# Kernel optimization log

Measured on AMD Instinct MI355X. Metric: run time of the kernel, lower is better.

## Reference

```python
import jax, jax.numpy as jnp
import numpy as np

H = 4          # attention heads
NEG_SLOPE = 0.2

def _gat_layer(h, src, dst, W, a_src, a_dst, b):
    # h: [N, F_in]; W: [F_in, H*D]; a_src/a_dst: [H, D]; b: [D]
    N = h.shape[0]
    D = a_src.shape[1]
    xh = (h @ W).reshape(N, H, D)                       # [N,H,D]
    al_src = jnp.einsum('nhd,hd->nh', xh, a_src)        # [N,H]
    al_dst = jnp.einsum('nhd,hd->nh', xh, a_dst)        # [N,H]
    e = jax.nn.leaky_relu(al_src[src] + al_dst[dst], NEG_SLOPE)  # [E,H]
    # segment softmax over incoming edges of each destination node
    m = jax.ops.segment_max(e, dst, num_segments=N)     # [N,H]
    ex = jnp.exp(e - m[dst])
    s = jax.ops.segment_sum(ex, dst, num_segments=N)
    alpha = ex / (s[dst] + 1e-16)                       # [E,H]
    out = jax.ops.segment_sum(xh[src] * alpha[:, :, None], dst, num_segments=N)  # [N,H,D]
    return out.mean(axis=1) + b                         # concat=False -> mean heads


def setup_inputs() -> dict:
    key = jax.random.key(0)
    ks = jax.random.split(key, 16)
    N, E, F_in, Dh = 50000, 400000, 128, 128
    inp = {
        'x': jax.random.normal(ks[0], (N, F_in), jnp.float32),
        'edge_index': jax.random.randint(ks[1], (2, E), 0, N, jnp.int64),
    }
    def glorot(k, shape):
        fan = shape[0] + shape[-1]
        return jax.random.uniform(k, shape, jnp.float32, -1.0, 1.0) * np.sqrt(6.0 / fan)
    dims = [F_in, Dh, Dh]
    for i, fin in enumerate(dims, start=1):
        inp[f'W{i}'] = glorot(ks[2 + 4 * i], (fin, H * Dh))
        inp[f'a_src{i}'] = glorot(ks[3 + 4 * i], (H, Dh))
        inp[f'a_dst{i}'] = glorot(ks[4 + 4 * i], (H, Dh))
        inp[f'b{i}'] = jnp.zeros((Dh,), jnp.float32)
    inp['Wp'] = glorot(ks[2], (Dh, Dh))
    inp['bp'] = jnp.zeros((Dh,), jnp.float32)
    return inp


def reference(x, edge_index, W1, a_src1, a_dst1, b1, W2, a_src2, a_dst2, b2,
              W3, a_src3, a_dst3, b3, Wp, bp):
    N = x.shape[0]
    loops = jnp.arange(N, dtype=edge_index.dtype)
    src = jnp.concatenate([edge_index[0], loops])   # GATConv adds self-loops
    dst = jnp.concatenate([edge_index[1], loops])
    h = x
    for W, a_s, a_d, b in ((W1, a_src1, a_dst1, b1),
                           (W2, a_src2, a_dst2, b2),
                           (W3, a_src3, a_dst3, b3)):
        h = _gat_layer(h, src, dst, W, a_s, a_d, b)
        h = jax.nn.relu(h)   # dropout is identity in eval mode
    return h @ Wp + bp
```

## Files before the change

kernel.cpp:

```cpp
#include <hip/hip_runtime.h>
#include <cstddef>
#include <cstdint>

typedef _Float16 half8 __attribute__((ext_vector_type(8)));
typedef float f32x4 __attribute__((ext_vector_type(4)));
typedef float f32x2 __attribute__((ext_vector_type(2)));
typedef unsigned short ushort_t;
typedef unsigned int uint_t;
typedef ushort_t ushort4v __attribute__((ext_vector_type(4)));
typedef float f32x4v __attribute__((ext_vector_type(4)));

#define INV_LN2 1.4426950408889634f

__device__ __forceinline__ ushort_t f_to_f16(float f) {
  _Float16 h = (_Float16)f;
  union { _Float16 h; ushort_t u; } v; v.h = h; return v.u;
}
__device__ __forceinline__ float f16_to_f(ushort_t u) {
  union { ushort_t u; _Float16 h; } v; v.u = u; return (float)v.h;
}

__global__ __launch_bounds__(64) void detect_i64_kernel(const int* __restrict__ ei,
                                                        int* __restrict__ flag) {
  if (threadIdx.x == 0) {
    int is32 = 0;
    for (int i = 1; i < 1001; i += 2) {
      if (ei[i] != 0) { is32 = 1; break; }
    }
    *flag = is32;
  }
}

__device__ __forceinline__ int load_src(const int* ei, int is32, int E, int e) {
  return is32 ? ei[e] : ei[2 * e];
}
__device__ __forceinline__ int load_dst(const int* ei, int is32, int E, int e) {
  return is32 ? ei[E + e] : ei[2 * (E + e)];
}

__global__ __launch_bounds__(256) void deg_kernel(const int* __restrict__ ei,
                                                  const int* __restrict__ flag,
                                                  int E, int N, int* __restrict__ deg) {
  int e = blockIdx.x * 256 + threadIdx.x;
  if (e >= E + N) return;
  int d = (e < E) ? load_dst(ei, *flag, E, e) : (e - E);
  atomicAdd(&deg[d], 1);
}

__global__ __launch_bounds__(256) void scan_blk_kernel(const int* __restrict__ deg,
                                                       int* __restrict__ rowptr,
                                                       int* __restrict__ bsum, int N) {
  __shared__ int buf[256];
  int b = blockIdx.x, t = threadIdx.x, i = b * 256 + t;
  int v = (i < N) ? deg[i] : 0;
  buf[t] = v;
  __syncthreads();
  for (int off = 1; off < 256; off <<= 1) {
    int add = (t >= off) ? buf[t - off] : 0;
    __syncthreads();
    buf[t] += add;
    __syncthreads();
  }
  if (i < N) rowptr[i + 1] = buf[t];
  if (t == 255) bsum[b] = buf[255];
  if (b == 0 && t == 0) rowptr[0] = 0;
}

__global__ __launch_bounds__(256) void scan_top_kernel(int* __restrict__ bsum, int NB) {
  __shared__ int buf[256];
  int t = threadIdx.x;
  int v = (t < NB) ? bsum[t] : 0;
  buf[t] = v;
  __syncthreads();
  for (int off = 1; off < 256; off <<= 1) {
    int add = (t >= off) ? buf[t - off] : 0;
    __syncthreads();
    buf[t] += add;
    __syncthreads();
  }
  if (t < NB) bsum[t] = buf[t];
}

__global__ __launch_bounds__(256) void scan_add_kernel(int* __restrict__ rowptr,
                                                       const int* __restrict__ bsum, int N) {
  int b = blockIdx.x, t = threadIdx.x, i = b * 256 + t;
  if (b > 0 && i < N) rowptr[i + 1] += bsum[b - 1];
}

__global__ __launch_bounds__(256) void fill_kernel(const int* __restrict__ ei,
                                                   const int* __restrict__ flag,
                                                   int E, int N,
                                                   const int* __restrict__ rowptr,
                                                   int* __restrict__ fillc,
                                                   int* __restrict__ colbuf) {
  int e = blockIdx.x * 256 + threadIdx.x;
  if (e >= E + N) return;
  int s, d;
  if (e < E) { int is32 = *flag; s = load_src(ei, is32, E, e); d = load_dst(ei, is32, E, e); }
  else { s = e - E; d = s; }
  int pos = atomicAdd(&fillc[d], 1);
  colbuf[rowptr[d] + pos] = s;
}

__global__ __launch_bounds__(256) void split_x16_kernel(const float* __restrict__ h,
                                                        ushort_t* __restrict__ h16,
                                                        int n) {
  int i = (blockIdx.x * 256 + threadIdx.x) * 4;
  if (i >= n) return;
  f32x4v v = *(const f32x4v*)&h[i];
  ushort4v s;
  s[0] = f_to_f16(v[0]); s[1] = f_to_f16(v[1]);
  s[2] = f_to_f16(v[2]); s[3] = f_to_f16(v[3]);
  *(ushort4v*)&h16[i] = s;
}

__global__ __launch_bounds__(256) void prep_weights_kernel(
    const float* __restrict__ W0, const float* __restrict__ W1,
    const float* __restrict__ W2, const float* __restrict__ Wp,
    ushort_t* __restrict__ wsf0, ushort_t* __restrict__ wsf1,
    ushort_t* __restrict__ wsf2, ushort_t* __restrict__ wpf) {
  int b = blockIdx.x;
  if (b < 768) {
    int L = b >> 8;
    const float* W = (L == 0) ? W0 : (L == 1) ? W1 : W2;
    ushort_t* out = (L == 0) ? wsf0 : (L == 1) ? wsf1 : wsf2;
    int t = (b & 255) * 256 + threadIdx.x;
    int c16 = t >> 13;
    int r = t & 8191;
    int k8 = r >> 7;
    int rem = r & 127;
    int rl = rem >> 3, kl = rem & 7;
    int col = c16 * 16 + rl;
    int k = k8 * 8 + kl;
    int h = k >> 7, f = k & 127;
    out[t] = f_to_f16(0.25f * W[(size_t)f * 512 + h * 128 + col]);
  } else {
    int t = (b - 768) * 256 + threadIdx.x;
    int blk = t >> 7, rem = t & 127;
    int c16 = blk >> 4, k8 = blk & 15;
    int cl = rem >> 3, kl = rem & 7;
    int col = c16 * 16 + cl, k = k8 * 8 + kl;
    wpf[t] = f_to_f16(Wp[(size_t)k * 128 + col]);
  }
}

__global__ __launch_bounds__(256) void wsd_kernel(const float* __restrict__ W,
                                                  const float* __restrict__ a_src,
                                                  const float* __restrict__ a_dst,
                                                  float* __restrict__ Ws4,
                                                  float* __restrict__ Wd4,
                                                  float* __restrict__ Wsh,
                                                  float* __restrict__ Wdh) {
  int wave = threadIdx.x >> 6, lane = threadIdx.x & 63;
  int f = blockIdx.x * 4 + wave;
  int base = lane * 8;
  float4 w0 = *(const float4*)&W[(size_t)f * 512 + base];
  float4 w1 = *(const float4*)&W[(size_t)f * 512 + base + 4];
  float4 s0 = *(const float4*)&a_src[base];
  float4 s1 = *(const float4*)&a_src[base + 4];
  float4 d0 = *(const float4*)&a_dst[base];
  float4 d1 = *(const float4*)&a_dst[base + 4];
  float ps = w0.x*s0.x + w0.y*s0.y + w0.z*s0.z + w0.w*s0.w
           + w1.x*s1.x + w1.y*s1.y + w1.z*s1.z + w1.w*s1.w;
  float pd = w0.x*d0.x + w0.y*d0.y + w0.z*d0.z + w0.w*d0.w
           + w1.x*d1.x + w1.y*d1.y + w1.z*d1.z + w1.w*d1.w;
#pragma unroll
  for (int off = 1; off <= 8; off <<= 1) {
    ps += __shfl_xor(ps, off);
    pd += __shfl_xor(pd, off);
  }
  if ((lane & 15) == 0) {
    int h = lane >> 4;
    float vs = ps * INV_LN2, vd = pd * INV_LN2;
    Ws4[f * 4 + h] = vs;
    Wd4[f * 4 + h] = vd;
    Wsh[h * 128 + f] = vs;
    Wdh[h * 128 + f] = vd;
  }
}

__global__ __launch_bounds__(256) void al_x_kernel(const float* __restrict__ x,
                                                   const float* __restrict__ Wsh,
                                                   const float* __restrict__ Wdh,
                                                   float* __restrict__ al_src,
                                                   float* __restrict__ al_dst, int N) {
  __shared__ float sWs[512], sWd[512];
  int t = threadIdx.x;
  sWs[t] = Wsh[t]; sWs[t + 256] = Wsh[t + 256];
  sWd[t] = Wdh[t]; sWd[t + 256] = Wdh[t + 256];
  __syncthreads();
  int wave = t >> 6, lane = t & 63;
  int n = blockIdx.x * 4 + wave;
  if (n >= N) return;
  float2 hv = *(const float2*)&x[(size_t)n * 128 + lane * 2];
  float p[8];
#pragma unroll
  for (int hh = 0; hh < 4; ++hh) {
    p[hh]     = hv.x * sWs[hh * 128 + 2 * lane] + hv.y * sWs[hh * 128 + 2 * lane + 1];
    p[4 + hh] = hv.x * sWd[hh * 128 + 2 * lane] + hv.y * sWd[hh * 128 + 2 * lane + 1];
  }
#pragma unroll
  for (int off = 32; off; off >>= 1)
#pragma unroll
    for (int i = 0; i < 8; ++i) p[i] += __shfl_xor(p[i], off);
  if (lane == 0) {
#pragma unroll
    for (int hh = 0; hh < 4; ++hh) {
      al_src[n * 4 + hh] = p[hh];
      al_dst[n * 4 + hh] = p[4 + hh];
    }
  }
}

__global__ __launch_bounds__(256) void agg_G_kernel(const ushort_t* __restrict__ h16,
                                                    const float* __restrict__ al_src,
                                                    const float* __restrict__ al_dst,
                                                    const int* __restrict__ rowptr,
                                                    const int* __restrict__ colbuf,
                                                    ushort_t* __restrict__ Gf, int N) {
  int wave = threadIdx.x >> 6, lane = threadIdx.x & 63;
  int hl = lane & 31;
  int half_base = lane & 32;
  int q = hl >> 2, hc = hl & 3;
  int qb = lane & ~3;
  int n = blockIdx.x * 8 + wave * 2 + (lane >> 5);
  bool alive = n < N;
  int beg = 0, d = 0;
  float ald_hc = 0.f;
  if (alive) {
    beg = rowptr[n];
    d = rowptr[n + 1] - beg;
    ald_hc = al_dst[(size_t)n * 4 + hc];
  }
  int dm1 = max(d - 1, 0);
  float m_run = -1e30f;
  f32x2 ss01 = {0.f, 0.f}, ss23 = {0.f, 0.f};
  f32x2 a0a = {0.f,0.f}, a0b = {0.f,0.f};
  f32x2 a1a = {0.f,0.f}, a1b = {0.f,0.f};
  f32x2 a2a = {0.f,0.f}, a2b = {0.f,0.f};
  f32x2 a3a = {0.f,0.f}, a3b = {0.f,0.f};

  for (int c0 = 0; c0 < d; c0 += 8) {
    int cn = min(8, d - c0);
    int j = c0 + q;
    int sq = colbuf[beg + min(j, dm1)];
    float e = al_src[(size_t)sq * 4 + hc] + ald_hc;
    e = fmaxf(e, 0.2f * e);
    e = (q < cn) ? e : -1e30f;
    float mc = e;
    mc = fmaxf(mc, __shfl_xor(mc, 4));
    mc = fmaxf(mc, __shfl_xor(mc, 8));
    mc = fmaxf(mc, __shfl_xor(mc, 16));
    float nm = fmaxf(m_run, mc);
    float fown = exp2f(m_run - nm);
    m_run = nm;
    float w_own = (q < cn) ? exp2f(e - nm) : 0.f;
    float f0 = __shfl(fown, qb + 0), f1 = __shfl(fown, qb + 1);
    float f2 = __shfl(fown, qb + 2), f3 = __shfl(fown, qb + 3);
    ss01 *= f32x2{f0, f1}; ss23 *= f32x2{f2, f3};
    f32x2 F0 = {f0, f0}, F1 = {f1, f1}, F2 = {f2, f2}, F3 = {f3, f3};
    a0a *= F0; a0b *= F0; a1a *= F1; a1b *= F1;
    a2a *= F2; a2b *= F2; a3a *= F3; a3b *= F3;
    int s_c = __shfl(sq, half_base);
    ushort4v hv_c = *(const ushort4v*)&h16[(size_t)s_c * 128 + hl * 4];
    for (int jj = 0; jj < cn; ++jj) {
      int s_n = __shfl(sq, half_base + min(jj + 1, cn - 1) * 4);
      ushort4v hv_n = *(const ushort4v*)&h16[(size_t)s_n * 128 + hl * 4];
      int wb = half_base + jj * 4;
      float w0 = __shfl(w_own, wb + 0);
      float w1 = __shfl(w_own, wb + 1);
      float w2 = __shfl(w_own, wb + 2);
      float w3 = __shfl(w_own, wb + 3);
      ss01 += f32x2{w0, w1}; ss23 += f32x2{w2, w3};
      f32x2 v01 = {f16_to_f(hv_c[0]), f16_to_f(hv_c[1])};
      f32x2 v23 = {f16_to_f(hv_c[2]), f16_to_f(hv_c[3])};
      a0a += f32x2{w0, w0} * v01; a0b += f32x2{w0, w0} * v23;
      a1a += f32x2{w1, w1} * v01; a1b += f32x2{w1, w1} * v23;
      a2a += f32x2{w2, w2} * v01; a2b += f32x2{w2, w2} * v23;
      a3a += f32x2{w3, w3} * v01; a3b += f32x2{w3, w3} * v23;
      hv_c = hv_n;
    }
  }
  if (!alive) return;
  float g[4][4];
  float inv;
  inv = 1.f / (ss01.x + 1e-16f);
  g[0][0] = a0a.x * inv; g[0][1] = a0a.y * inv; g[0][2] = a0b.x * inv; g[0][3] = a0b.y * inv;
  inv = 1.f / (ss01.y + 1e-16f);
  g[1][0] = a1a.x * inv; g[1][1] = a1a.y * inv; g[1][2] = a1b.x * inv; g[1][3] = a1b.y * inv;
  inv = 1.f / (ss23.x + 1e-16f);
  g[2][0] = a2a.x * inv; g[2][1] = a2a.y * inv; g[2][2] = a2b.x * inv; g[2][3] = a2b.y * inv;
  inv = 1.f / (ss23.y + 1e-16f);
  g[3][0] = a3a.x * inv; g[3][1] = a3a.y * inv; g[3][2] = a3b.x * inv; g[3][3] = a3b.y * inv;
#pragma unroll
  for (int h = 0; h < 4; ++h) {
    ushort_t q0 = f_to_f16(g[h][0]), q1 = f_to_f16(g[h][1]);
    ushort_t q2 = f_to_f16(g[h][2]), q3 = f_to_f16(g[h][3]);
    size_t o = ((size_t)(n >> 4) * 64 + h * 16 + (hl >> 1)) * 128 + (n & 15) * 8 + (hl & 1) * 4;
    *(uint2*)&Gf[o] = make_uint2((uint_t)q0 | ((uint_t)q1 << 16),
                                 (uint_t)q2 | ((uint_t)q3 << 16));
  }
}

template <int K, int MODE>
__global__ __launch_bounds__(256) void gemm_frag_kernel(
    const ushort_t* __restrict__ Af, const ushort_t* __restrict__ Bf,
    ushort_t* __restrict__ H16, ushort_t* __restrict__ Cf16, float* __restrict__ Cf,
    const float* __restrict__ WsN, const float* __restrict__ WdN,
    float* __restrict__ alS, float* __restrict__ alD,
    int M, const float* __restrict__ bias) {
  constexpr int KT = K >> 5;
  constexpr int KTH = KT >> 1;
  constexpr int PS = 16 * K;
  __shared__ float lacc[2][8][4][64];
  int lane = threadIdx.x & 63;
  int wv = threadIdx.x >> 6;
  int pair = wv >> 1, khalf = wv & 1;
  int wid = blockIdx.x * 2 + pair;
  int krow = lane >> 4, ml = lane & 15;
  int lb = krow * 128 + ml * 8;
  size_t abase = (size_t)wid * PS + lb + (size_t)khalf * KTH * 512;
  size_t bbase = (size_t)lb + (size_t)khalf * KTH * 512;
  f32x4 acc[8] = {};
  half8 a_c = *(const half8*)&Af[abase];
  half8 b_c[8];
#pragma unroll
  for (int j = 0; j < 8; ++j) b_c[j] = *(const half8*)&Bf[j * PS + bbase];
#pragma unroll
  for (int kt = 0; kt < KTH; ++kt) {
    half8 a_n = a_c;
    half8 b_n[8];
#pragma unroll
    for (int j = 0; j < 8; ++j) b_n[j] = b_c[j];
    if (kt + 1 < KTH) {
      a_n = *(const half8*)&Af[abase + (kt + 1) * 512];
#pragma unroll
      for (int j = 0; j < 8; ++j)
        b_n[j] = *(const half8*)&Bf[j * PS + bbase + (kt + 1) * 512];
    }
#pragma unroll
    for (int j = 0; j < 8; ++j)
      acc[j] = __builtin_amdgcn_mfma_f32_16x16x32_f16(a_c, b_c[j], acc[j], 0, 0, 0);
    a_c = a_n;
#pragma unroll
    for (int j = 0; j < 8; ++j) b_c[j] = b_n[j];
  }
  if (khalf == 1) {
#pragma unroll
    for (int j = 0; j < 8; ++j)
#pragma unroll
      for (int c = 0; c < 4; ++c) lacc[pair][j][c][lane] = acc[j][c];
  }
  __syncthreads();
  if (khalf == 1) return;
#pragma unroll
  for (int j = 0; j < 8; ++j)
#pragma unroll
    for (int c = 0; c < 4; ++c) acc[j][c] += lacc[pair][j][c][lane];

  int wrow0 = wid * 16;
  if (MODE == 0) {
    float ps[4][4] = {};
    float pd[4][4] = {};
#pragma unroll
    for (int j = 0; j < 8; ++j) {
      int col = j * 16 + ml;
      float bv = bias[col];
      float4 w4s = *(const float4*)&WsN[col * 4];
      float4 w4d = *(const float4*)&WdN[col * 4];
#pragma unroll
      for (int r = 0; r < 4; ++r) {
        int row = wrow0 + krow * 4 + r;
        float v = fmaxf(acc[j][r] + bv, 0.f);
        if (row < M) H16[(size_t)row * 128 + col] = f_to_f16(v);
        ps[0][r] += v * w4s.x; ps[1][r] += v * w4s.y;
        ps[2][r] += v * w4s.z; ps[3][r] += v * w4s.w;
        pd[0][r] += v * w4d.x; pd[1][r] += v * w4d.y;
        pd[2][r] += v * w4d.z; pd[3][r] += v * w4d.w;
      }
    }
#pragma unroll
    for (int off = 1; off <= 8; off <<= 1) {
#pragma unroll
      for (int hh = 0; hh < 4; ++hh)
#pragma unroll
        for (int r = 0; r < 4; ++r) {
          ps[hh][r] += __shfl_xor(ps[hh][r], off);
          pd[hh][r] += __shfl_xor(pd[hh][r], off);
        }
    }
    if (ml == 0) {
#pragma unroll
      for (int r = 0; r < 4; ++r) {
        int row = wrow0 + krow * 4 + r;
        if (row < M) {
#pragma unroll
          for (int hh = 0; hh < 4; ++hh) {
            alS[row * 4 + hh] = ps[hh][r];
            alD[row * 4 + hh] = pd[hh][r];
          }
        }
      }
    }
  } else {
#pragma unroll
    for (int j = 0; j < 8; ++j) {
      int col = j * 16 + ml;
      float bv = bias[col];
#pragma unroll
      for (int r = 0; r < 4; ++r) {
        int row = wrow0 + krow * 4 + r;
        if (row < M) {
          float v = acc[j][r] + bv;
          if (MODE != 2) v = fmaxf(v, 0.f);
          if (MODE == 1) {
            size_t o = ((size_t)(row >> 4) * 16 + (col >> 3)) * 128 + (row & 15) * 8 + (col & 7);
            Cf16[o] = f_to_f16(v);
          } else {
            Cf[(size_t)row * 128 + col] = v;
          }
        }
      }
    }
  }
}

extern "C" void kernel_launch(void* const* d_in, const int* in_sizes, int n_in,
                              void* d_out, int out_size, void* d_ws, size_t ws_size,
                              hipStream_t stream) {
  const float* x  = (const float*)d_in[0];
  const int*   ei = (const int*)d_in[1];
  const float* Wl[3]  = {(const float*)d_in[2], (const float*)d_in[6], (const float*)d_in[10]};
  const float* asr[3] = {(const float*)d_in[3], (const float*)d_in[7], (const float*)d_in[11]};
  const float* adr[3] = {(const float*)d_in[4], (const float*)d_in[8], (const float*)d_in[12]};
  const float* bl[3]  = {(const float*)d_in[5], (const float*)d_in[9], (const float*)d_in[13]};
  const float* Wp = (const float*)d_in[14];
  const float* bp = (const float*)d_in[15];

  const int N = in_sizes[0] / 128;
  const int E = in_sizes[1] / 2;
  const int EN = E + N;
  const int Mtiles = (N + 127) / 128;
  const int Mp = Mtiles * 128;
  const int NB = (N + 255) / 256;
  const int NPB2 = Mp / 16 / 2;

  char* ws = (char*)d_ws;
  size_t off = 0;
  auto carve = [&](size_t bytes) -> void* {
    void* p = ws + off;
    off = (off + bytes + 255) & ~(size_t)255;
    return p;
  };
  ushort_t* Gf    = (ushort_t*)carve((size_t)Mp * 512 * 2);
  ushort_t* h16   = (ushort_t*)carve((size_t)N * 128 * 2);
  ushort_t* h3f   = (ushort_t*)carve((size_t)Mp * 128 * 2);
  ushort_t* wsf0  = (ushort_t*)carve((size_t)128 * 512 * 2);
  ushort_t* wsf1  = (ushort_t*)carve((size_t)128 * 512 * 2);
  ushort_t* wsf2  = (ushort_t*)carve((size_t)128 * 512 * 2);
  ushort_t* wpf   = (ushort_t*)carve((size_t)128 * 128 * 2);
  float*    alsrc = (float*)carve((size_t)N * 4 * 4);
  float*    aldst = (float*)carve((size_t)N * 4 * 4);
  float*    Ws4   = (float*)carve(3 * 512 * 4);
  float*    Wd4   = (float*)carve(3 * 512 * 4);
  float*    Wsh   = (float*)carve(3 * 512 * 4);
  float*    Wdh   = (float*)carve(3 * 512 * 4);
  int*      rowptr= (int*)carve((size_t)(N + 1) * 4);
  int*      deg   = (int*)carve((size_t)N * 4);
  int*      bsum  = (int*)carve(256 * 4);
  int*      fillc = (int*)carve((size_t)N * 4);
  int*      colbuf= (int*)carve((size_t)EN * 4);
  int*      flag  = (int*)carve(256);

  detect_i64_kernel<<<1, 64, 0, stream>>>(ei, flag);
  hipMemsetAsync(deg, 0, (size_t)N * 4, stream);
  hipMemsetAsync(fillc, 0, (size_t)N * 4, stream);
  int ebl = (EN + 255) / 256;
  deg_kernel<<<ebl, 256, 0, stream>>>(ei, flag, E, N, deg);
  scan_blk_kernel<<<NB, 256, 0, stream>>>(deg, rowptr, bsum, N);
  scan_top_kernel<<<1, 256, 0, stream>>>(bsum, NB);
  scan_add_kernel<<<NB, 256, 0, stream>>>(rowptr, bsum, N);
  fill_kernel<<<ebl, 256, 0, stream>>>(ei, flag, E, N, rowptr, fillc, colbuf);

  const int n_real = N * 128;
  split_x16_kernel<<<(n_real / 4 + 255) / 256, 256, 0, stream>>>(x, h16, n_real);
  prep_weights_kernel<<<832, 256, 0, stream>>>(Wl[0], Wl[1], Wl[2], Wp,
                                               wsf0, wsf1, wsf2, wpf);
  for (int L = 0; L < 3; ++L)
    wsd_kernel<<<32, 256, 0, stream>>>(Wl[L], asr[L], adr[L],
                                       Ws4 + L * 512, Wd4 + L * 512,
                                       Wsh + L * 512, Wdh + L * 512);
  al_x_kernel<<<(N + 3) / 4, 256, 0, stream>>>(x, Wsh, Wdh, alsrc, aldst, N);

  ushort_t* wsfL[3] = {wsf0, wsf1, wsf2};
  for (int L = 0; L < 3; ++L) {
    agg_G_kernel<<<Mp / 8, 256, 0, stream>>>(h16, alsrc, aldst,
                                             rowptr, colbuf, Gf, N);
    if (L < 2) {
      gemm_frag_kernel<512, 0><<<NPB2, 256, 0, stream>>>(Gf, wsfL[L],
                                                         h16, nullptr, nullptr,
                                                         Ws4 + (L + 1) * 512, Wd4 + (L + 1) * 512,
                                                         alsrc, aldst, N, bl[L]);
    } else {
      gemm_frag_kernel<512, 1><<<NPB2, 256, 0, stream>>>(Gf, wsfL[L],
                                                         nullptr, h3f, nullptr,
                                                         nullptr, nullptr, nullptr, nullptr,
                                                         N, bl[L]);
    }
  }

  gemm_frag_kernel<128, 2><<<NPB2, 256, 0, stream>>>(h3f, wpf,
                                                     nullptr, nullptr, (float*)d_out,
                                                     nullptr, nullptr, nullptr, nullptr,
                                                     N, bp);
}
```

Baseline: 312.8 us.

## Fuse edge aggregation with per-layer GEMM via shared-memory G tile

Merges the aggregation kernel and the per-layer GEMM into one kernel. Each 512-thread block aggregates 16 nodes into an XOR-swizzled shared-memory tile, then each of its 8 waves computes 16 output columns with MFMA. Attention logits for the next layer are reduced through shared memory. The input and output feature and logit buffers are ping-ponged, since other blocks still read neighbours while outputs are written. This removes the global write and read of the 50000x512 fp16 G buffer and a launch per layer, but each block reloads the full weight matrix and the GEMM tile gets smaller.

```diff
diff --git a/kernel.cpp b/kernel.cpp
--- a/kernel.cpp
+++ b/kernel.cpp
@@ -212,18 +212,27 @@
   }
 }
 
-__global__ __launch_bounds__(256) void agg_G_kernel(const ushort_t* __restrict__ h16,
-                                                    const float* __restrict__ al_src,
-                                                    const float* __restrict__ al_dst,
-                                                    const int* __restrict__ rowptr,
-                                                    const int* __restrict__ colbuf,
-                                                    ushort_t* __restrict__ Gf, int N) {
+template <int MODE>
+__global__ __launch_bounds__(512) void layer_fused_kernel(
+    const ushort_t* __restrict__ h16in,
+    const float* __restrict__ al_src, const float* __restrict__ al_dst,
+    const int* __restrict__ rowptr, const int* __restrict__ colbuf,
+    const ushort_t* __restrict__ Bf,
+    ushort_t* __restrict__ h16out,
+    const float* __restrict__ WsN, const float* __restrict__ WdN,
+    float* __restrict__ alSo, float* __restrict__ alDo,
+    ushort_t* __restrict__ Cf16,
+    int N, const float* __restrict__ bias) {
+  constexpr int PS = 16 * 512;
+  __shared__ ushort_t Gs[16 * 512];
+  __shared__ float alred[8][16][8];
   int wave = threadIdx.x >> 6, lane = threadIdx.x & 63;
   int hl = lane & 31;
   int half_base = lane & 32;
   int q = hl >> 2, hc = hl & 3;
   int qb = lane & ~3;
-  int n = blockIdx.x * 8 + wave * 2 + (lane >> 5);
+  int nloc = wave * 2 + (lane >> 5);
+  int n = blockIdx.x * 16 + nloc;
   bool alive = n < N;
   int beg = 0, d = 0;
   float ald_hc = 0.f;
@@ -262,10 +271,10 @@
     a0a *= F0; a0b *= F0; a1a *= F1; a1b *= F1;
     a2a *= F2; a2b *= F2; a3a *= F3; a3b *= F3;
     int s_c = __shfl(sq, half_base);
-    ushort4v hv_c = *(const ushort4v*)&h16[(size_t)s_c * 128 + hl * 4];
+    ushort4v hv_c = *(const ushort4v*)&h16in[(size_t)s_c * 128 + hl * 4];
     for (int jj = 0; jj < cn; ++jj) {
       int s_n = __shfl(sq, half_base + min(jj + 1, cn - 1) * 4);
-      ushort4v hv_n = *(const ushort4v*)&h16[(size_t)s_n * 128 + hl * 4];
+      ushort4v hv_n = *(const ushort4v*)&h16in[(size_t)s_n * 128 + hl * 4];
       int wb = half_base + jj * 4;
       float w0 = __shfl(w_own, wb + 0);
       float w1 = __shfl(w_own, wb + 1);
@@ -281,36 +290,114 @@
       hv_c = hv_n;
     }
   }
-  if (!alive) return;
-  float g[4][4];
-  float inv;
-  inv = 1.f / (ss01.x + 1e-16f);
-  g[0][0] = a0a.x * inv; g[0][1] = a0a.y * inv; g[0][2] = a0b.x * inv; g[0][3] = a0b.y * inv;
-  inv = 1.f / (ss01.y + 1e-16f);
-  g[1][0] = a1a.x * inv; g[1][1] = a1a.y * inv; g[1][2] = a1b.x * inv; g[1][3] = a1b.y * inv;
-  inv = 1.f / (ss23.x + 1e-16f);
-  g[2][0] = a2a.x * inv; g[2][1] = a2a.y * inv; g[2][2] = a2b.x * inv; g[2][3] = a2b.y * inv;
-  inv = 1.f / (ss23.y + 1e-16f);
-  g[3][0] = a3a.x * inv; g[3][1] = a3a.y * inv; g[3][2] = a3b.x * inv; g[3][3] = a3b.y * inv;
-#pragma unroll
-  for (int h = 0; h < 4; ++h) {
-    ushort_t q0 = f_to_f16(g[h][0]), q1 = f_to_f16(g[h][1]);
-    ushort_t q2 = f_to_f16(g[h][2]), q3 = f_to_f16(g[h][3]);
-    size_t o = ((size_t)(n >> 4) * 64 + h * 16 + (hl >> 1)) * 128 + (n & 15) * 8 + (hl & 1) * 4;
-    *(uint2*)&Gf[o] = make_uint2((uint_t)q0 | ((uint_t)q1 << 16),
-                                 (uint_t)q2 | ((uint_t)q3 << 16));
-  }
-}
-
-template <int K, int MODE>
-__global__ __launch_bounds__(256) void gemm_frag_kernel(
+  {
+    float g[4][4];
+    float inv;
+    inv = 1.f / (ss01.x + 1e-16f);
+    g[0][0] = a0a.x * inv; g[0][1] = a0a.y * inv; g[0][2] = a0b.x * inv; g[0][3] = a0b.y * inv;
+    inv = 1.f / (ss01.y + 1e-16f);
+    g[1][0] = a1a.x * inv; g[1][1] = a1a.y * inv; g[1][2] = a1b.x * inv; g[1][3] = a1b.y * inv;
+    inv = 1.f / (ss23.x + 1e-16f);
+    g[2][0] = a2a.x * inv; g[2][1] = a2a.y * inv; g[2][2] = a2b.x * inv; g[2][3] = a2b.y * inv;
+    inv = 1.f / (ss23.y + 1e-16f);
+    g[3][0] = a3a.x * inv; g[3][1] = a3a.y * inv; g[3][2] = a3b.x * inv; g[3][3] = a3b.y * inv;
+#pragma unroll
+    for (int h = 0; h < 4; ++h) {
+      ushort_t q0 = f_to_f16(g[h][0]), q1 = f_to_f16(g[h][1]);
+      ushort_t q2 = f_to_f16(g[h][2]), q3 = f_to_f16(g[h][3]);
+      int k8 = h * 16 + (hl >> 1);
+      int slot = nloc ^ ((hl >> 1) & 7);
+      int o = k8 * 128 + slot * 8 + (hl & 1) * 4;
+      *(uint2*)&Gs[o] = make_uint2((uint_t)q0 | ((uint_t)q1 << 16),
+                                   (uint_t)q2 | ((uint_t)q3 << 16));
+    }
+  }
+  if (MODE == 0) {
+    ((float*)alred)[threadIdx.x] = 0.f;
+    ((float*)alred)[threadIdx.x + 512] = 0.f;
+  }
+  int krow = lane >> 4, ml = lane & 15;
+  int lb = krow * 128 + ml * 8;
+  const ushort_t* Bw = Bf + (size_t)wave * PS;
+  half8 b[8];
+#pragma unroll
+  for (int i = 0; i < 8; ++i) b[i] = *(const half8*)&Bw[i * 512 + lb];
+  __syncthreads();
+
+  f32x4 acc = {0.f, 0.f, 0.f, 0.f};
+#pragma unroll
+  for (int kt = 0; kt < 16; ++kt) {
+    half8 bb = b[kt & 7];
+    if (kt < 8) b[kt] = *(const half8*)&Bw[(kt + 8) * 512 + lb];
+    int k8 = kt * 4 + krow;
+    half8 a = *(const half8*)&Gs[k8 * 128 + (ml ^ (k8 & 7)) * 8];
+    acc = __builtin_amdgcn_mfma_f32_16x16x32_f16(a, bb, acc, 0, 0, 0);
+  }
+  int col = wave * 16 + ml;
+  float bv = bias[col];
+  int rbase = blockIdx.x * 16 + krow * 4;
+  if (MODE == 0) {
+    float4 w4s = *(const float4*)&WsN[col * 4];
+    float4 w4d = *(const float4*)&WdN[col * 4];
+    float vr[4];
+    float ps[4][4], pd[4][4];
+#pragma unroll
+    for (int r = 0; r < 4; ++r) {
+      vr[r] = fmaxf(acc[r] + bv, 0.f);
+      int row = rbase + r;
+      if (row < N) h16out[(size_t)row * 128 + col] = f_to_f16(vr[r]);
+      ps[0][r] = vr[r] * w4s.x; ps[1][r] = vr[r] * w4s.y;
+      ps[2][r] = vr[r] * w4s.z; ps[3][r] = vr[r] * w4s.w;
+      pd[0][r] = vr[r] * w4d.x; pd[1][r] = vr[r] * w4d.y;
+      pd[2][r] = vr[r] * w4d.z; pd[3][r] = vr[r] * w4d.w;
+    }
+#pragma unroll
+    for (int off = 1; off <= 8; off <<= 1) {
+#pragma unroll
+      for (int hh = 0; hh < 4; ++hh)
+#pragma unroll
+        for (int r = 0; r < 4; ++r) {
+          ps[hh][r] += __shfl_xor(ps[hh][r], off);
+          pd[hh][r] += __shfl_xor(pd[hh][r], off);
+        }
+    }
+    if (ml == 0) {
+#pragma unroll
+      for (int r = 0; r < 4; ++r)
+#pragma unroll
+        for (int hh = 0; hh < 4; ++hh) {
+          alred[wave][krow * 4 + r][hh] = ps[hh][r];
+          alred[wave][krow * 4 + r][4 + hh] = pd[hh][r];
+        }
+    }
+    __syncthreads();
+    if (threadIdx.x < 128) {
+      int lr = threadIdx.x >> 3, k = threadIdx.x & 7;
+      float s = 0.f;
+#pragma unroll
+      for (int w = 0; w < 8; ++w) s += alred[w][lr][k];
+      int row = blockIdx.x * 16 + lr;
+      if (row < N) {
+        if (k < 4) alSo[row * 4 + k] = s;
+        else       alDo[row * 4 + (k - 4)] = s;
+      }
+    }
+  } else {
+#pragma unroll
+    for (int r = 0; r < 4; ++r) {
+      float v = fmaxf(acc[r] + bv, 0.f);
+      size_t o = ((size_t)blockIdx.x * 16 + wave * 2 + (ml >> 3)) * 128
+               + (krow * 4 + r) * 8 + (ml & 7);
+      Cf16[o] = f_to_f16(v);
+    }
+  }
+}
+
+__global__ __launch_bounds__(256) void proj_kernel(
     const ushort_t* __restrict__ Af, const ushort_t* __restrict__ Bf,
-    ushort_t* __restrict__ H16, ushort_t* __restrict__ Cf16, float* __restrict__ Cf,
-    const float* __restrict__ WsN, const float* __restrict__ WdN,
-    float* __restrict__ alS, float* __restrict__ alD,
-    int M, const float* __restrict__ bias) {
-  constexpr int KT = K >> 5;
-  constexpr int KTH = KT >> 1;
+    float* __restrict__ Cf, int M, const float* __restrict__ bias) {
+  constexpr int K = 128;
+  constexpr int KTH = 2;
   constexpr int PS = 16 * K;
   __shared__ float lacc[2][8][4][64];
   int lane = threadIdx.x & 63;
@@ -322,28 +409,14 @@
   size_t abase = (size_t)wid * PS + lb + (size_t)khalf * KTH * 512;
   size_t bbase = (size_t)lb + (size_t)khalf * KTH * 512;
   f32x4 acc[8] = {};
-  half8 a_c = *(const half8*)&Af[abase];
-  half8 b_c[8];
-#pragma unroll
-  for (int j = 0; j < 8; ++j) b_c[j] = *(const half8*)&Bf[j * PS + bbase];
 #pragma unroll
   for (int kt = 0; kt < KTH; ++kt) {
-    half8 a_n = a_c;
-    half8 b_n[8];
-#pragma unroll
-    for (int j = 0; j < 8; ++j) b_n[j] = b_c[j];
-    if (kt + 1 < KTH) {
-      a_n = *(const half8*)&Af[abase + (kt + 1) * 512];
-#pragma unroll
-      for (int j = 0; j < 8; ++j)
-        b_n[j] = *(const half8*)&Bf[j * PS + bbase + (kt + 1) * 512];
-    }
-#pragma unroll
-    for (int j = 0; j < 8; ++j)
-      acc[j] = __builtin_amdgcn_mfma_f32_16x16x32_f16(a_c, b_c[j], acc[j], 0, 0, 0);
-    a_c = a_n;
-#pragma unroll
-    for (int j = 0; j < 8; ++j) b_c[j] = b_n[j];
+    half8 a = *(const half8*)&Af[abase + kt * 512];
+#pragma unroll
+    for (int j = 0; j < 8; ++j) {
+      half8 bb = *(const half8*)&Bf[j * PS + bbase + kt * 512];
+      acc[j] = __builtin_amdgcn_mfma_f32_16x16x32_f16(a, bb, acc[j], 0, 0, 0);
+    }
   }
   if (khalf == 1) {
 #pragma unroll
@@ -357,70 +430,15 @@
   for (int j = 0; j < 8; ++j)
 #pragma unroll
     for (int c = 0; c < 4; ++c) acc[j][c] += lacc[pair][j][c][lane];
-
   int wrow0 = wid * 16;
-  if (MODE == 0) {
-    float ps[4][4] = {};
-    float pd[4][4] = {};
-#pragma unroll
-    for (int j = 0; j < 8; ++j) {
-      int col = j * 16 + ml;
-      float bv = bias[col];
-      float4 w4s = *(const float4*)&WsN[col * 4];
-      float4 w4d = *(const float4*)&WdN[col * 4];
-#pragma unroll
-      for (int r = 0; r < 4; ++r) {
-        int row = wrow0 + krow * 4 + r;
-        float v = fmaxf(acc[j][r] + bv, 0.f);
-        if (row < M) H16[(size_t)row * 128 + col] = f_to_f16(v);
-        ps[0][r] += v * w4s.x; ps[1][r] += v * w4s.y;
-        ps[2][r] += v * w4s.z; ps[3][r] += v * w4s.w;
-        pd[0][r] += v * w4d.x; pd[1][r] += v * w4d.y;
-        pd[2][r] += v * w4d.z; pd[3][r] += v * w4d.w;
-      }
-    }
-#pragma unroll
-    for (int off = 1; off <= 8; off <<= 1) {
-#pragma unroll
-      for (int hh = 0; hh < 4; ++hh)
-#pragma unroll
-        for (int r = 0; r < 4; ++r) {
-          ps[hh][r] += __shfl_xor(ps[hh][r], off);
-          pd[hh][r] += __shfl_xor(pd[hh][r], off);
-        }
-    }
-    if (ml == 0) {
-#pragma unroll
-      for (int r = 0; r < 4; ++r) {
-        int row = wrow0 + krow * 4 + r;
-        if (row < M) {
-#pragma unroll
-          for (int hh = 0; hh < 4; ++hh) {
-            alS[row * 4 + hh] = ps[hh][r];
-            alD[row * 4 + hh] = pd[hh][r];
-          }
-        }
-      }
-    }
-  } else {
-#pragma unroll
-    for (int j = 0; j < 8; ++j) {
-      int col = j * 16 + ml;
-      float bv = bias[col];
-#pragma unroll
-      for (int r = 0; r < 4; ++r) {
-        int row = wrow0 + krow * 4 + r;
-        if (row < M) {
-          float v = acc[j][r] + bv;
-          if (MODE != 2) v = fmaxf(v, 0.f);
-          if (MODE == 1) {
-            size_t o = ((size_t)(row >> 4) * 16 + (col >> 3)) * 128 + (row & 15) * 8 + (col & 7);
-            Cf16[o] = f_to_f16(v);
-          } else {
-            Cf[(size_t)row * 128 + col] = v;
-          }
-        }
-      }
+#pragma unroll
+  for (int j = 0; j < 8; ++j) {
+    int col = j * 16 + ml;
+    float bv = bias[col];
+#pragma unroll
+    for (int r = 0; r < 4; ++r) {
+      int row = wrow0 + krow * 4 + r;
+      if (row < M) Cf[(size_t)row * 128 + col] = acc[j][r] + bv;
     }
   }
 }
@@ -443,7 +461,8 @@
   const int Mtiles = (N + 127) / 128;
   const int Mp = Mtiles * 128;
   const int NB = (N + 255) / 256;
-  const int NPB2 = Mp / 16 / 2;
+  const int NPAN = Mp / 16;
+  const int NPB2 = NPAN / 2;
 
   char* ws = (char*)d_ws;
   size_t off = 0;
@@ -452,15 +471,17 @@
     off = (off + bytes + 255) & ~(size_t)255;
     return p;
   };
-  ushort_t* Gf    = (ushort_t*)carve((size_t)Mp * 512 * 2);
-  ushort_t* h16   = (ushort_t*)carve((size_t)N * 128 * 2);
+  ushort_t* h16A  = (ushort_t*)carve((size_t)N * 128 * 2);
+  ushort_t* h16B  = (ushort_t*)carve((size_t)N * 128 * 2);
   ushort_t* h3f   = (ushort_t*)carve((size_t)Mp * 128 * 2);
   ushort_t* wsf0  = (ushort_t*)carve((size_t)128 * 512 * 2);
   ushort_t* wsf1  = (ushort_t*)carve((size_t)128 * 512 * 2);
   ushort_t* wsf2  = (ushort_t*)carve((size_t)128 * 512 * 2);
   ushort_t* wpf   = (ushort_t*)carve((size_t)128 * 128 * 2);
-  float*    alsrc = (float*)carve((size_t)N * 4 * 4);
-  float*    aldst = (float*)carve((size_t)N * 4 * 4);
+  float*    alsA  = (float*)carve((size_t)N * 4 * 4);
+  float*    aldA  = (float*)carve((size_t)N * 4 * 4);
+  float*    alsB  = (float*)carve((size_t)N * 4 * 4);
+  float*    aldB  = (float*)carve((size_t)N * 4 * 4);
   float*    Ws4   = (float*)carve(3 * 512 * 4);
   float*    Wd4   = (float*)carve(3 * 512 * 4);
   float*    Wsh   = (float*)carve(3 * 512 * 4);
@@ -483,34 +504,27 @@
   fill_kernel<<<ebl, 256, 0, stream>>>(ei, flag, E, N, rowptr, fillc, colbuf);
 
   const int n_real = N * 128;
-  split_x16_kernel<<<(n_real / 4 + 255) / 256, 256, 0, stream>>>(x, h16, n_real);
+  split_x16_kernel<<<(n_real / 4 + 255) / 256, 256, 0, stream>>>(x, h16A, n_real);
   prep_weights_kernel<<<832, 256, 0, stream>>>(Wl[0], Wl[1], Wl[2], Wp,
                                                wsf0, wsf1, wsf2, wpf);
   for (int L = 0; L < 3; ++L)
     wsd_kernel<<<32, 256, 0, stream>>>(Wl[L], asr[L], adr[L],
                                        Ws4 + L * 512, Wd4 + L * 512,
                                        Wsh + L * 512, Wdh + L * 512);
-  al_x_kernel<<<(N + 3) / 4, 256, 0, stream>>>(x, Wsh, Wdh, alsrc, aldst, N);
-
-  ushort_t* wsfL[3] = {wsf0, wsf1, wsf2};
-  for (int L = 0; L < 3; ++L) {
-    agg_G_kernel<<<Mp / 8, 256, 0, stream>>>(h16, alsrc, aldst,
-                                             rowptr, colbuf, Gf, N);
-    if (L < 2) {
-      gemm_frag_kernel<512, 0><<<NPB2, 256, 0, stream>>>(Gf, wsfL[L],
-                                                         h16, nullptr, nullptr,
-                                                         Ws4 + (L + 1) * 512, Wd4 + (L + 1) * 512,
-                                                         alsrc, aldst, N, bl[L]);
-    } else {
-      gemm_frag_kernel<512, 1><<<NPB2, 256, 0, stream>>>(Gf, wsfL[L],
-                                                         nullptr, h3f, nullptr,
-                                                         nullptr, nullptr, nullptr, nullptr,
-                                                         N, bl[L]);
-    }
-  }
-
-  gemm_frag_kernel<128, 2><<<NPB2, 256, 0, stream>>>(h3f, wpf,
-                                                     nullptr, nullptr, (float*)d_out,
-                                                     nullptr, nullptr, nullptr, nullptr,
-                                                     N, bp);
-}
+  al_x_kernel<<<(N + 3) / 4, 256, 0, stream>>>(x, Wsh, Wdh, alsA, aldA, N);
+
+  layer_fused_kernel<0><<<NPAN, 512, 0, stream>>>(h16A, alsA, aldA, rowptr, colbuf,
+                                                  wsf0, h16B,
+                                                  Ws4 + 512, Wd4 + 512, alsB, aldB,
+                                                  nullptr, N, bl[0]);
+  layer_fused_kernel<0><<<NPAN, 512, 0, stream>>>(h16B, alsB, aldB, rowptr, colbuf,
+                                                  wsf1, h16A,
+                                                  Ws4 + 1024, Wd4 + 1024, alsA, aldA,
+                                                  nullptr, N, bl[1]);
+  layer_fused_kernel<1><<<NPAN, 512, 0, stream>>>(h16A, alsA, aldA, rowptr, colbuf,
+                                                  wsf2, nullptr,
+                                                  nullptr, nullptr, nullptr, nullptr,
+                                                  h3f, N, bl[2]);
+
+  proj_kernel<<<NPB2, 256, 0, stream>>>(h3f, wpf, (float*)d_out, N, bp);
+}
```

After: 333.5 us. 6.6% more time.
